# Kernel tuning notes

Measured on AMD Instinct MI355X. Metric: run time of the kernel, lower is better.

## Reference

```python
import jax, jax.numpy as jnp
import numpy as np

B, S, D, H, DFF = 2, 2048, 768, 12, 3072
DH = D // H
EPS = 1e-5


def _ln(x, g, b):
    m = jnp.mean(x, axis=-1, keepdims=True)
    v = jnp.mean((x - m) ** 2, axis=-1, keepdims=True)
    return (x - m) * jax.lax.rsqrt(v + EPS) * g + b


def setup_inputs() -> dict:
    key = jax.random.key(0)
    ks = jax.random.split(key, 13)
    sd = 1.0 / np.sqrt(D)
    sf = 1.0 / np.sqrt(DFF)
    return {
        "x": jax.random.normal(ks[0], (B, S, D), jnp.float32),
        "Wq": jax.random.uniform(ks[1], (D, D), jnp.float32, -sd, sd),
        "bq": jnp.zeros((D,), jnp.float32),
        "Wk": jax.random.uniform(ks[2], (D, D), jnp.float32, -sd, sd),
        "bk": jnp.zeros((D,), jnp.float32),
        "Wv": jax.random.uniform(ks[3], (D, D), jnp.float32, -sd, sd),
        "bv": jnp.zeros((D,), jnp.float32),
        "Wo": jax.random.uniform(ks[4], (D, D), jnp.float32, -sd, sd),
        "bo": jnp.zeros((D,), jnp.float32),
        "W1": jax.random.uniform(ks[5], (D, DFF), jnp.float32, -sd, sd),
        "b1": jnp.zeros((DFF,), jnp.float32),
        "W2": jax.random.uniform(ks[6], (DFF, D), jnp.float32, -sf, sf),
        "b2": jnp.zeros((D,), jnp.float32),
        "g1": jnp.ones((D,), jnp.float32),
        "be1": jnp.zeros((D,), jnp.float32),
        "g2": jnp.ones((D,), jnp.float32),
        "be2": jnp.zeros((D,), jnp.float32),
    }


def reference(x, Wq, bq, Wk, bk, Wv, bv, Wo, bo, W1, b1, W2, b2, g1, be1, g2, be2):
    # QKV projections, then split heads: [B,S,D] -> [B,H,S,DH]
    def heads(t):
        return t.reshape(B, S, H, DH).transpose(0, 2, 1, 3)
    Q = heads(x @ Wq + bq)
    K = heads(x @ Wk + bk)
    V = heads(x @ Wv + bv)
    # Per-head loop in original == batched-over-heads attention here (same math)
    scores = jnp.einsum("bhqd,bhkd->bhqk", Q, K) / np.sqrt(DH)
    attn = jax.nn.softmax(scores, axis=-1)  # [B,H,S,S] -- dominant intermediate
    ctx = jnp.einsum("bhqk,bhkd->bhqd", attn, V)
    ctx = ctx.transpose(0, 2, 1, 3).reshape(B, S, D)  # concat heads
    x = x + (ctx @ Wo + bo)
    x = _ln(x, g1, be1)
    ffn = (jax.nn.gelu(x @ W1 + b1, approximate=False)) @ W2 + b2
    x = _ln(x + ffn, g2, be2)
    return x
```

## Files before the change

kernel.cpp:

```cpp
#include <hip/hip_runtime.h>
#include <math.h>

#define BB 2
#define SS 2048
#define DD 768
#define HH 12
#define DHH 64
#define DFFN 3072
#define MTOK (BB*SS)

typedef __attribute__((ext_vector_type(8))) __bf16 bf16x8;
typedef __attribute__((ext_vector_type(4))) float f32x4;

__device__ __forceinline__ unsigned short f2bf(float f) {
    unsigned int b = __builtin_bit_cast(unsigned int, f);
    b += 0x7FFFu + ((b >> 16) & 1u);
    return (unsigned short)(b >> 16);
}

__device__ __forceinline__ void gload_lds16(const void* g, void* l) {
    __builtin_amdgcn_global_load_lds((const __attribute__((address_space(1))) unsigned int*)g,
                                     (__attribute__((address_space(3))) unsigned int*)l,
                                     16, 0, 0);
}

template <int ACT, int OBF>
__global__ __launch_bounds__(256) void gemm_mfma(const unsigned short* __restrict__ A,
                                                 const unsigned short* __restrict__ Bt,
                                                 const float* __restrict__ bias,
                                                 void* __restrict__ Cout,
                                                 int M, int N, int K) {
    __shared__ unsigned short As[128 * 64];
    __shared__ unsigned short Bs[128 * 64];
    const int tid = threadIdx.x;
    const int lane = tid & 63;
    const int w = tid >> 6;
    const int l15 = lane & 15, l4 = lane >> 4;
    const int m0 = blockIdx.x * 128;
    const int n0 = blockIdx.y * 128;
    const int wr = (w >> 1) * 64;
    const int wc = (w & 1) * 64;

    f32x4 acc[4][4] = {};

    int srow[4], scd[4];
#pragma unroll
    for (int i = 0; i < 4; ++i) {
        int s = w * 256 + i * 64 + lane;
        srow[i] = s >> 3;
        scd[i] = (((s & 7) ^ (srow[i] & 7))) * 8;
    }

    for (int k0 = 0; k0 < K; k0 += 64) {
        __syncthreads();
#pragma unroll
        for (int i = 0; i < 4; ++i) {
            const unsigned short* gA = A + (size_t)(m0 + srow[i]) * K + k0 + scd[i];
            gload_lds16(gA, &As[(w * 256 + i * 64) * 8]);
        }
#pragma unroll
        for (int i = 0; i < 4; ++i) {
            const unsigned short* gB = Bt + (size_t)(n0 + srow[i]) * K + k0 + scd[i];
            gload_lds16(gB, &Bs[(w * 256 + i * 64) * 8]);
        }
        __syncthreads();
#pragma unroll
        for (int ks = 0; ks < 2; ++ks) {
            bf16x8 af[4], bfr[4];
#pragma unroll
            for (int m = 0; m < 4; ++m) {
                int r = wr + m * 16 + l15;
                int c = (ks * 4 + l4) ^ (r & 7);
                af[m] = *(const bf16x8*)&As[(r * 8 + c) * 8];
            }
#pragma unroll
            for (int n = 0; n < 4; ++n) {
                int r = wc + n * 16 + l15;
                int c = (ks * 4 + l4) ^ (r & 7);
                bfr[n] = *(const bf16x8*)&Bs[(r * 8 + c) * 8];
            }
#pragma unroll
            for (int m = 0; m < 4; ++m)
#pragma unroll
                for (int n = 0; n < 4; ++n)
                    acc[m][n] = __builtin_amdgcn_mfma_f32_16x16x32_bf16(af[m], bfr[n], acc[m][n], 0, 0, 0);
        }
    }

#pragma unroll
    for (int n = 0; n < 4; ++n) {
        int col = n0 + wc + n * 16 + l15;
        float bv = bias[col];
#pragma unroll
        for (int m = 0; m < 4; ++m) {
#pragma unroll
            for (int r = 0; r < 4; ++r) {
                int row = m0 + wr + m * 16 + l4 * 4 + r;
                float v = acc[m][n][r] + bv;
                if (ACT) v = 0.5f * v * (1.0f + erff(v * 0.70710678118654752f));
                if (OBF) ((unsigned short*)Cout)[(size_t)row * N + col] = f2bf(v);
                else     ((float*)Cout)[(size_t)row * N + col] = v;
            }
        }
    }
}

__global__ __launch_bounds__(256) void attn_mfma(const unsigned short* __restrict__ QKV,
                                                 const unsigned short* __restrict__ Vt,
                                                 unsigned short* __restrict__ Ctx) {
    __shared__ unsigned short Ks[64 * 64];
    __shared__ unsigned short Vs[64 * 64];
    __shared__ unsigned short Ps[4 * 1024];
    const int tid = threadIdx.x;
    const int lane = tid & 63;
    const int w = tid >> 6;
    const int l15 = lane & 15, l4 = lane >> 4;
    const int bh = blockIdx.y;
    const int b = bh / HH, h = bh % HH;
    const int q0 = blockIdx.x * 64;
    unsigned short* pw = Ps + w * 1024;

    bf16x8 qf[2];
    {
        int qr = b * SS + q0 + w * 16 + l15;
        const unsigned short* qp = QKV + (size_t)qr * 2304 + h * 64 + l4 * 8;
        qf[0] = *(const bf16x8*)qp;
        qf[1] = *(const bf16x8*)(qp + 32);
    }

    f32x4 oacc[4] = {};
    float m_run[4], l_run[4];
#pragma unroll
    for (int r = 0; r < 4; ++r) { m_run[r] = -1e30f; l_run[r] = 0.0f; }

    int arow[2], acd[2];
#pragma unroll
    for (int i = 0; i < 2; ++i) {
        int s = w * 128 + i * 64 + lane;
        arow[i] = s >> 3;
        acd[i] = ((s & 7) ^ (arow[i] & 7)) * 8;
    }

    for (int kt = 0; kt < SS / 64; ++kt) {
        const int k0 = kt * 64;
        __syncthreads();
#pragma unroll
        for (int i = 0; i < 2; ++i) {
            const unsigned short* gK = QKV + (size_t)(b * SS + k0 + arow[i]) * 2304 + DD + h * 64 + acd[i];
            gload_lds16(gK, &Ks[(w * 128 + i * 64) * 8]);
        }
#pragma unroll
        for (int i = 0; i < 2; ++i) {
            const unsigned short* gV = Vt + (size_t)(bh * 64 + arow[i]) * SS + k0 + acd[i];
            gload_lds16(gV, &Vs[(w * 128 + i * 64) * 8]);
        }
        __syncthreads();

        f32x4 s4[4] = {};
#pragma unroll
        for (int ks = 0; ks < 2; ++ks) {
#pragma unroll
            for (int n = 0; n < 4; ++n) {
                int r = n * 16 + l15;
                int c = (ks * 4 + l4) ^ (r & 7);
                bf16x8 kf = *(const bf16x8*)&Ks[(r * 8 + c) * 8];
                s4[n] = __builtin_amdgcn_mfma_f32_16x16x32_bf16(qf[ks], kf, s4[n], 0, 0, 0);
            }
        }

        float p[4][4];
        float corr[4];
#pragma unroll
        for (int r = 0; r < 4; ++r) {
            float mt = fmaxf(fmaxf(s4[0][r], s4[1][r]), fmaxf(s4[2][r], s4[3][r])) * 0.125f;
#pragma unroll
            for (int off = 1; off < 16; off <<= 1) mt = fmaxf(mt, __shfl_xor(mt, off));
            float mn = fmaxf(m_run[r], mt);
            corr[r] = __expf(m_run[r] - mn);
            float rs = 0.0f;
#pragma unroll
            for (int n = 0; n < 4; ++n) {
                float pv = __expf(s4[n][r] * 0.125f - mn);
                p[n][r] = pv; rs += pv;
            }
#pragma unroll
            for (int off = 1; off < 16; off <<= 1) rs += __shfl_xor(rs, off);
            l_run[r] = l_run[r] * corr[r] + rs;
            m_run[r] = mn;
        }
#pragma unroll
        for (int n = 0; n < 4; ++n)
#pragma unroll
            for (int r = 0; r < 4; ++r) oacc[n][r] *= corr[r];

#pragma unroll
        for (int n = 0; n < 4; ++n) {
            int col = n * 16 + l15;
#pragma unroll
            for (int r = 0; r < 4; ++r) {
                int q = l4 * 4 + r;
                int byte = q * 128 + (((col >> 3) ^ (q & 7)) * 16) + (col & 7) * 2;
                *(unsigned short*)((char*)pw + byte) = f2bf(p[n][r]);
            }
        }

#pragma unroll
        for (int ks = 0; ks < 2; ++ks) {
            int cpa = (ks * 4 + l4) ^ (l15 & 7);
            bf16x8 pa = *(const bf16x8*)((const char*)pw + l15 * 128 + cpa * 16);
#pragma unroll
            for (int n = 0; n < 4; ++n) {
                int r = n * 16 + l15;
                int c = (ks * 4 + l4) ^ (r & 7);
                bf16x8 vf = *(const bf16x8*)&Vs[(r * 8 + c) * 8];
                oacc[n] = __builtin_amdgcn_mfma_f32_16x16x32_bf16(pa, vf, oacc[n], 0, 0, 0);
            }
        }
    }

#pragma unroll
    for (int n = 0; n < 4; ++n) {
        int col = h * 64 + n * 16 + l15;
#pragma unroll
        for (int r = 0; r < 4; ++r) {
            int q = b * SS + q0 + w * 16 + l4 * 4 + r;
            Ctx[(size_t)q * DD + col] = f2bf(oacc[n][r] / l_run[r]);
        }
    }
}

__global__ __launch_bounds__(256) void v_transpose(const unsigned short* __restrict__ QKV,
                                                   unsigned short* __restrict__ Vt) {
    __shared__ unsigned short t[64][66];
    const int tid = threadIdx.x;
    const int bh = blockIdx.y, b = bh / HH, h = bh % HH;
    const int s0 = blockIdx.x * 64;
    const int c = tid & 63, r0 = tid >> 6;
#pragma unroll
    for (int i = 0; i < 16; ++i) {
        int r = i * 4 + r0;
        t[r][c] = QKV[(size_t)(b * SS + s0 + r) * 2304 + 1536 + h * 64 + c];
    }
    __syncthreads();
#pragma unroll
    for (int i = 0; i < 16; ++i) {
        int r = i * 4 + r0;
        Vt[((size_t)bh * 64 + r) * SS + s0 + c] = t[c][r];
    }
}

__global__ __launch_bounds__(256) void wtrans(const float* __restrict__ W,
                                              unsigned short* __restrict__ Wt,
                                              int K, int N, int rowoff) {
    __shared__ float t[32][33];
    const int tid = threadIdx.x;
    const int k0 = blockIdx.x * 32, n0 = blockIdx.y * 32;
    const int c = tid & 31, r0 = tid >> 5;
#pragma unroll
    for (int i = 0; i < 4; ++i) {
        int r = i * 8 + r0;
        t[r][c] = W[(size_t)(k0 + r) * N + n0 + c];
    }
    __syncthreads();
#pragma unroll
    for (int i = 0; i < 4; ++i) {
        int r = i * 8 + r0;
        Wt[(size_t)(rowoff + n0 + r) * K + k0 + c] = f2bf(t[c][r]);
    }
}

__global__ __launch_bounds__(256) void f2b_vec(const float* __restrict__ in,
                                               unsigned short* __restrict__ out, int n4) {
    int i = blockIdx.x * 256 + threadIdx.x;
    if (i < n4) {
        float4 v = ((const float4*)in)[i];
        unsigned long long pk = (unsigned long long)f2bf(v.x)
                              | ((unsigned long long)f2bf(v.y) << 16)
                              | ((unsigned long long)f2bf(v.z) << 32)
                              | ((unsigned long long)f2bf(v.w) << 48);
        ((unsigned long long*)out)[i] = pk;
    }
}

__global__ __launch_bounds__(256) void bias_concat(const float* __restrict__ q,
                                                   const float* __restrict__ k,
                                                   const float* __restrict__ v,
                                                   float* __restrict__ o) {
    int i = blockIdx.x * 256 + threadIdx.x;
    if (i < DD) { o[i] = q[i]; o[DD + i] = k[i]; o[2 * DD + i] = v[i]; }
}

template <int WB>
__global__ __launch_bounds__(256) void add_ln(const float* __restrict__ a,
                                              const float* __restrict__ bsrc,
                                              const float* __restrict__ g,
                                              const float* __restrict__ be,
                                              float* __restrict__ outf,
                                              unsigned short* __restrict__ outb) {
    const int row = blockIdx.x;
    const int tid = threadIdx.x;
    float x[3];
    float s = 0.0f, s2 = 0.0f;
#pragma unroll
    for (int i = 0; i < 3; ++i) {
        int c = tid + i * 256;
        float v = a[(size_t)row * DD + c] + bsrc[(size_t)row * DD + c];
        x[i] = v; s += v; s2 += v * v;
    }
#pragma unroll
    for (int off = 32; off; off >>= 1) {
        s += __shfl_down(s, off);
        s2 += __shfl_down(s2, off);
    }
    __shared__ float ws[8];
    const int wid = tid >> 6, lane = tid & 63;
    if (lane == 0) { ws[wid] = s; ws[4 + wid] = s2; }
    __syncthreads();
    if (tid == 0) {
        ws[0] = ws[0] + ws[1] + ws[2] + ws[3];
        ws[4] = ws[4] + ws[5] + ws[6] + ws[7];
    }
    __syncthreads();
    const float mean = ws[0] * (1.0f / DD);
    const float var = ws[4] * (1.0f / DD) - mean * mean;
    const float inv = rsqrtf(var + 1e-5f);
#pragma unroll
    for (int i = 0; i < 3; ++i) {
        int c = tid + i * 256;
        float res = (x[i] - mean) * inv * g[c] + be[c];
        outf[(size_t)row * DD + c] = res;
        if (WB) outb[(size_t)row * DD + c] = f2bf(res);
    }
}

extern "C" void kernel_launch(void* const* d_in, const int* in_sizes, int n_in,
                              void* d_out, int out_size, void* d_ws, size_t ws_size,
                              hipStream_t stream) {
    const float* x   = (const float*)d_in[0];
    const float* Wq  = (const float*)d_in[1];
    const float* bq  = (const float*)d_in[2];
    const float* Wk  = (const float*)d_in[3];
    const float* bk  = (const float*)d_in[4];
    const float* Wv  = (const float*)d_in[5];
    const float* bv  = (const float*)d_in[6];
    const float* Wo  = (const float*)d_in[7];
    const float* bo  = (const float*)d_in[8];
    const float* W1  = (const float*)d_in[9];
    const float* b1  = (const float*)d_in[10];
    const float* W2  = (const float*)d_in[11];
    const float* b2  = (const float*)d_in[12];
    const float* g1  = (const float*)d_in[13];
    const float* be1 = (const float*)d_in[14];
    const float* g2  = (const float*)d_in[15];
    const float* be2 = (const float*)d_in[16];
    float* out = (float*)d_out;

    char* w8 = (char*)d_ws;
    unsigned short* QKV = (unsigned short*)w8;
    unsigned short* Vt  = (unsigned short*)(w8 + 18874368);
    unsigned short* Hff = (unsigned short*)w8;
    char* p = w8 + 25165824;
    unsigned short* Ctxb  = (unsigned short*)p; p += 6291456;
    unsigned short* xb    = (unsigned short*)p; p += 6291456;
    unsigned short* Wqkvt = (unsigned short*)p; p += 3538944;
    unsigned short* Wot   = (unsigned short*)p; p += 1179648;
    unsigned short* W1t   = (unsigned short*)p; p += 4718592;
    unsigned short* W2t   = (unsigned short*)p; p += 4718592;
    float* bqkv = (float*)p; p += 9216 + 256;
    float* Proj = (float*)p; p += 12582912;
    float* X2   = (float*)p; p += 12582912;

    dim3 blk(256);

    f2b_vec<<<dim3(3072), blk, 0, stream>>>(x, xb, MTOK * DD / 4);
    wtrans<<<dim3(24, 24), blk, 0, stream>>>(Wq, Wqkvt, DD, DD, 0);
    wtrans<<<dim3(24, 24), blk, 0, stream>>>(Wk, Wqkvt, DD, DD, DD);
    wtrans<<<dim3(24, 24), blk, 0, stream>>>(Wv, Wqkvt, DD, DD, 2 * DD);
    wtrans<<<dim3(24, 24), blk, 0, stream>>>(Wo, Wot, DD, DD, 0);
    wtrans<<<dim3(24, 96), blk, 0, stream>>>(W1, W1t, DD, DFFN, 0);
    wtrans<<<dim3(96, 24), blk, 0, stream>>>(W2, W2t, DFFN, DD, 0);
    bias_concat<<<dim3(3), blk, 0, stream>>>(bq, bk, bv, bqkv);

    gemm_mfma<0, 1><<<dim3(32, 18), blk, 0, stream>>>(xb, Wqkvt, bqkv, QKV, MTOK, 3 * DD, DD);
    v_transpose<<<dim3(32, 24), blk, 0, stream>>>(QKV, Vt);
    attn_mfma<<<dim3(32, 24), blk, 0, stream>>>(QKV, Vt, Ctxb);
    gemm_mfma<0, 0><<<dim3(32, 6), blk, 0, stream>>>(Ctxb, Wot, bo, Proj, MTOK, DD, DD);
    add_ln<1><<<dim3(MTOK), blk, 0, stream>>>(x, Proj, g1, be1, X2, xb);
    gemm_mfma<1, 1><<<dim3(32, 24), blk, 0, stream>>>(xb, W1t, b1, Hff, MTOK, DFFN, DD);
    gemm_mfma<0, 0><<<dim3(32, 6), blk, 0, stream>>>(Hff, W2t, b2, Proj, MTOK, DD, DFFN);
    add_ln<0><<<dim3(MTOK), blk, 0, stream>>>(X2, Proj, g2, be2, out, nullptr);
}
```

Measured before the change: 381.9 us.

## Use 32x32 MFMA flash attention with register P; split-K output GEMMs

The attention kernel is rewritten to use 32x32x16 MFMA with 32 query rows per wave and 128 queries per block. Computing S^T lets the P matrix stay in registers, moved between lanes with cross-half shuffles instead of an LDS round-trip, and softmax uses exp2 with the scale folded in. The Wo and W2 GEMMs are split along K into two launches writing separate fp32 partials. Those partials are summed with the bias inside a new three-input add+LayerNorm kernel. The split aims to fill more CUs for the narrow N=768 GEMMs, at the cost of an extra partial-buffer write and read.

```diff
diff --git a/kernel.cpp b/kernel.cpp
--- a/kernel.cpp
+++ b/kernel.cpp
@@ -11,6 +11,7 @@
 
 typedef __attribute__((ext_vector_type(8))) __bf16 bf16x8;
 typedef __attribute__((ext_vector_type(4))) float f32x4;
+typedef __attribute__((ext_vector_type(16))) float f32x16;
 
 __device__ __forceinline__ unsigned short f2bf(float f) {
     unsigned int b = __builtin_bit_cast(unsigned int, f);
@@ -29,7 +30,7 @@
                                                  const unsigned short* __restrict__ Bt,
                                                  const float* __restrict__ bias,
                                                  void* __restrict__ Cout,
-                                                 int M, int N, int K) {
+                                                 int M, int N, int ldA, int ldB, int Klen) {
     __shared__ unsigned short As[128 * 64];
     __shared__ unsigned short Bs[128 * 64];
     const int tid = threadIdx.x;
@@ -51,16 +52,16 @@
         scd[i] = (((s & 7) ^ (srow[i] & 7))) * 8;
     }
 
-    for (int k0 = 0; k0 < K; k0 += 64) {
+    for (int k0 = 0; k0 < Klen; k0 += 64) {
         __syncthreads();
 #pragma unroll
         for (int i = 0; i < 4; ++i) {
-            const unsigned short* gA = A + (size_t)(m0 + srow[i]) * K + k0 + scd[i];
+            const unsigned short* gA = A + (size_t)(m0 + srow[i]) * ldA + k0 + scd[i];
             gload_lds16(gA, &As[(w * 256 + i * 64) * 8]);
         }
 #pragma unroll
         for (int i = 0; i < 4; ++i) {
-            const unsigned short* gB = Bt + (size_t)(n0 + srow[i]) * K + k0 + scd[i];
+            const unsigned short* gB = Bt + (size_t)(n0 + srow[i]) * ldB + k0 + scd[i];
             gload_lds16(gB, &Bs[(w * 256 + i * 64) * 8]);
         }
         __syncthreads();
@@ -90,7 +91,7 @@
 #pragma unroll
     for (int n = 0; n < 4; ++n) {
         int col = n0 + wc + n * 16 + l15;
-        float bv = bias[col];
+        float bv = bias ? bias[col] : 0.0f;
 #pragma unroll
         for (int m = 0; m < 4; ++m) {
 #pragma unroll
@@ -105,33 +106,32 @@
     }
 }
 
-__global__ __launch_bounds__(256) void attn_mfma(const unsigned short* __restrict__ QKV,
-                                                 const unsigned short* __restrict__ Vt,
-                                                 unsigned short* __restrict__ Ctx) {
+__global__ __launch_bounds__(256) void attn_mfma2(const unsigned short* __restrict__ QKV,
+                                                  const unsigned short* __restrict__ Vt,
+                                                  unsigned short* __restrict__ Ctx) {
     __shared__ unsigned short Ks[64 * 64];
     __shared__ unsigned short Vs[64 * 64];
-    __shared__ unsigned short Ps[4 * 1024];
     const int tid = threadIdx.x;
     const int lane = tid & 63;
     const int w = tid >> 6;
-    const int l15 = lane & 15, l4 = lane >> 4;
+    const int l31 = lane & 31;
+    const int hi = lane >> 5;
     const int bh = blockIdx.y;
     const int b = bh / HH, h = bh % HH;
-    const int q0 = blockIdx.x * 64;
-    unsigned short* pw = Ps + w * 1024;
-
-    bf16x8 qf[2];
+    const int q0 = blockIdx.x * 128 + w * 32;
+    const float CLOG = 0.18033688011112042f;
+
+    bf16x8 qf[4];
     {
-        int qr = b * SS + q0 + w * 16 + l15;
-        const unsigned short* qp = QKV + (size_t)qr * 2304 + h * 64 + l4 * 8;
+        const unsigned short* qp = QKV + (size_t)(b * SS + q0 + l31) * 2304 + h * 64 + hi * 8;
         qf[0] = *(const bf16x8*)qp;
-        qf[1] = *(const bf16x8*)(qp + 32);
-    }
-
-    f32x4 oacc[4] = {};
-    float m_run[4], l_run[4];
-#pragma unroll
-    for (int r = 0; r < 4; ++r) { m_run[r] = -1e30f; l_run[r] = 0.0f; }
+        qf[1] = *(const bf16x8*)(qp + 16);
+        qf[2] = *(const bf16x8*)(qp + 32);
+        qf[3] = *(const bf16x8*)(qp + 48);
+    }
+
+    f32x16 oacc[2] = {};
+    float m_run = -1e30f, l_run = 0.0f;
 
     int arow[2], acd[2];
 #pragma unroll
@@ -156,75 +156,93 @@
         }
         __syncthreads();
 
-        f32x4 s4[4] = {};
-#pragma unroll
-        for (int ks = 0; ks < 2; ++ks) {
-#pragma unroll
-            for (int n = 0; n < 4; ++n) {
-                int r = n * 16 + l15;
-                int c = (ks * 4 + l4) ^ (r & 7);
-                bf16x8 kf = *(const bf16x8*)&Ks[(r * 8 + c) * 8];
-                s4[n] = __builtin_amdgcn_mfma_f32_16x16x32_bf16(qf[ks], kf, s4[n], 0, 0, 0);
-            }
-        }
-
-        float p[4][4];
-        float corr[4];
-#pragma unroll
-        for (int r = 0; r < 4; ++r) {
-            float mt = fmaxf(fmaxf(s4[0][r], s4[1][r]), fmaxf(s4[2][r], s4[3][r])) * 0.125f;
-#pragma unroll
-            for (int off = 1; off < 16; off <<= 1) mt = fmaxf(mt, __shfl_xor(mt, off));
-            float mn = fmaxf(m_run[r], mt);
-            corr[r] = __expf(m_run[r] - mn);
-            float rs = 0.0f;
-#pragma unroll
-            for (int n = 0; n < 4; ++n) {
-                float pv = __expf(s4[n][r] * 0.125f - mn);
-                p[n][r] = pv; rs += pv;
-            }
-#pragma unroll
-            for (int off = 1; off < 16; off <<= 1) rs += __shfl_xor(rs, off);
-            l_run[r] = l_run[r] * corr[r] + rs;
-            m_run[r] = mn;
-        }
-#pragma unroll
-        for (int n = 0; n < 4; ++n)
-#pragma unroll
-            for (int r = 0; r < 4; ++r) oacc[n][r] *= corr[r];
-
-#pragma unroll
-        for (int n = 0; n < 4; ++n) {
-            int col = n * 16 + l15;
-#pragma unroll
-            for (int r = 0; r < 4; ++r) {
-                int q = l4 * 4 + r;
-                int byte = q * 128 + (((col >> 3) ^ (q & 7)) * 16) + (col & 7) * 2;
-                *(unsigned short*)((char*)pw + byte) = f2bf(p[n][r]);
-            }
-        }
-
-#pragma unroll
-        for (int ks = 0; ks < 2; ++ks) {
-            int cpa = (ks * 4 + l4) ^ (l15 & 7);
-            bf16x8 pa = *(const bf16x8*)((const char*)pw + l15 * 128 + cpa * 16);
-#pragma unroll
-            for (int n = 0; n < 4; ++n) {
-                int r = n * 16 + l15;
-                int c = (ks * 4 + l4) ^ (r & 7);
-                bf16x8 vf = *(const bf16x8*)&Vs[(r * 8 + c) * 8];
-                oacc[n] = __builtin_amdgcn_mfma_f32_16x16x32_bf16(pa, vf, oacc[n], 0, 0, 0);
-            }
-        }
-    }
-
-#pragma unroll
-    for (int n = 0; n < 4; ++n) {
-        int col = h * 64 + n * 16 + l15;
-#pragma unroll
-        for (int r = 0; r < 4; ++r) {
-            int q = b * SS + q0 + w * 16 + l4 * 4 + r;
-            Ctx[(size_t)q * DD + col] = f2bf(oacc[n][r] / l_run[r]);
+        f32x16 st[2] = {};
+#pragma unroll
+        for (int t = 0; t < 2; ++t) {
+#pragma unroll
+            for (int ks = 0; ks < 4; ++ks) {
+                int row = 32 * t + l31;
+                int ch = (2 * ks + hi) ^ (row & 7);
+                bf16x8 kf = *(const bf16x8*)&Ks[(row * 8 + ch) * 8];
+                st[t] = __builtin_amdgcn_mfma_f32_32x32x16_bf16(kf, qf[ks], st[t], 0, 0, 0);
+            }
+        }
+
+        float pmax = st[0][0];
+#pragma unroll
+        for (int r = 1; r < 16; ++r) pmax = fmaxf(pmax, st[0][r]);
+#pragma unroll
+        for (int r = 0; r < 16; ++r) pmax = fmaxf(pmax, st[1][r]);
+        pmax = fmaxf(pmax, __shfl_xor(pmax, 32));
+        pmax *= CLOG;
+        const float mn = fmaxf(m_run, pmax);
+        const float corr = exp2f(m_run - mn);
+
+        unsigned int Wn[2][4][2];
+        float rs = 0.0f;
+#pragma unroll
+        for (int t = 0; t < 2; ++t) {
+#pragma unroll
+            for (int blk = 0; blk < 4; ++blk) {
+                float pa = exp2f(fmaf(st[t][4 * blk + 0], CLOG, -mn));
+                float pb = exp2f(fmaf(st[t][4 * blk + 1], CLOG, -mn));
+                float pc = exp2f(fmaf(st[t][4 * blk + 2], CLOG, -mn));
+                float pd = exp2f(fmaf(st[t][4 * blk + 3], CLOG, -mn));
+                rs += (pa + pb) + (pc + pd);
+                Wn[t][blk][0] = (unsigned int)f2bf(pa) | ((unsigned int)f2bf(pb) << 16);
+                Wn[t][blk][1] = (unsigned int)f2bf(pc) | ((unsigned int)f2bf(pd) << 16);
+            }
+        }
+        rs += __shfl_xor(rs, 32);
+        l_run = l_run * corr + rs;
+        m_run = mn;
+
+#pragma unroll
+        for (int d = 0; d < 2; ++d)
+#pragma unroll
+            for (int r = 0; r < 16; ++r) oacc[d][r] *= corr;
+
+        unsigned int PW[2][4][2];
+#pragma unroll
+        for (int t = 0; t < 2; ++t)
+#pragma unroll
+            for (int blk = 0; blk < 4; ++blk)
+#pragma unroll
+                for (int u = 0; u < 2; ++u) PW[t][blk][u] = __shfl_xor(Wn[t][blk][u], 32);
+
+        const bool h1 = (hi == 1);
+#pragma unroll
+        for (int t = 0; t < 2; ++t) {
+#pragma unroll
+            for (int ks2 = 0; ks2 < 2; ++ks2) {
+                union { unsigned int u[4]; bf16x8 v; } pu;
+                pu.u[0] = h1 ? PW[t][2 * ks2 + 1][0] : Wn[t][2 * ks2][0];
+                pu.u[1] = h1 ? PW[t][2 * ks2 + 1][1] : Wn[t][2 * ks2][1];
+                pu.u[2] = h1 ? Wn[t][2 * ks2 + 1][0] : PW[t][2 * ks2][0];
+                pu.u[3] = h1 ? Wn[t][2 * ks2 + 1][1] : PW[t][2 * ks2][1];
+#pragma unroll
+                for (int d = 0; d < 2; ++d) {
+                    int row = 32 * d + l31;
+                    int ch = (4 * t + 2 * ks2 + hi) ^ (row & 7);
+                    bf16x8 vf = *(const bf16x8*)&Vs[(row * 8 + ch) * 8];
+                    oacc[d] = __builtin_amdgcn_mfma_f32_32x32x16_bf16(vf, pu.v, oacc[d], 0, 0, 0);
+                }
+            }
+        }
+    }
+
+    const float inv = 1.0f / l_run;
+    unsigned short* cp = Ctx + (size_t)(b * SS + q0 + l31) * DD + h * 64;
+#pragma unroll
+    for (int d = 0; d < 2; ++d) {
+#pragma unroll
+        for (int blk = 0; blk < 4; ++blk) {
+            unsigned long long pk =
+                  (unsigned long long)f2bf(oacc[d][4 * blk + 0] * inv)
+                | ((unsigned long long)f2bf(oacc[d][4 * blk + 1] * inv) << 16)
+                | ((unsigned long long)f2bf(oacc[d][4 * blk + 2] * inv) << 32)
+                | ((unsigned long long)f2bf(oacc[d][4 * blk + 3] * inv) << 48);
+            *(unsigned long long*)(cp + 32 * d + 8 * blk + 4 * hi) = pk;
         }
     }
 }
@@ -291,12 +309,14 @@
 }
 
 template <int WB>
-__global__ __launch_bounds__(256) void add_ln(const float* __restrict__ a,
-                                              const float* __restrict__ bsrc,
-                                              const float* __restrict__ g,
-                                              const float* __restrict__ be,
-                                              float* __restrict__ outf,
-                                              unsigned short* __restrict__ outb) {
+__global__ __launch_bounds__(256) void add_ln3(const float* __restrict__ a,
+                                               const float* __restrict__ p1,
+                                               const float* __restrict__ p2,
+                                               const float* __restrict__ bias,
+                                               const float* __restrict__ g,
+                                               const float* __restrict__ be,
+                                               float* __restrict__ outf,
+                                               unsigned short* __restrict__ outb) {
     const int row = blockIdx.x;
     const int tid = threadIdx.x;
     float x[3];
@@ -304,7 +324,8 @@
 #pragma unroll
     for (int i = 0; i < 3; ++i) {
         int c = tid + i * 256;
-        float v = a[(size_t)row * DD + c] + bsrc[(size_t)row * DD + c];
+        size_t idx = (size_t)row * DD + c;
+        float v = a[idx] + p1[idx] + p2[idx] + bias[c];
         x[i] = v; s += v; s2 += v * v;
     }
 #pragma unroll
@@ -357,18 +378,18 @@
 
     char* w8 = (char*)d_ws;
     unsigned short* QKV = (unsigned short*)w8;
+    unsigned short* Hff = (unsigned short*)w8;
     unsigned short* Vt  = (unsigned short*)(w8 + 18874368);
-    unsigned short* Hff = (unsigned short*)w8;
-    char* p = w8 + 25165824;
-    unsigned short* Ctxb  = (unsigned short*)p; p += 6291456;
-    unsigned short* xb    = (unsigned short*)p; p += 6291456;
-    unsigned short* Wqkvt = (unsigned short*)p; p += 3538944;
-    unsigned short* Wot   = (unsigned short*)p; p += 1179648;
-    unsigned short* W1t   = (unsigned short*)p; p += 4718592;
-    unsigned short* W2t   = (unsigned short*)p; p += 4718592;
-    float* bqkv = (float*)p; p += 9216 + 256;
-    float* Proj = (float*)p; p += 12582912;
-    float* X2   = (float*)p; p += 12582912;
+    unsigned short* Ctxb  = (unsigned short*)(w8 + 25165824);
+    unsigned short* xb    = (unsigned short*)(w8 + 31457280);
+    unsigned short* Wqkvt = (unsigned short*)(w8 + 37748736);
+    unsigned short* Wot   = (unsigned short*)(w8 + 41287680);
+    unsigned short* W1t   = (unsigned short*)(w8 + 42467328);
+    unsigned short* W2t   = (unsigned short*)(w8 + 47185920);
+    float* bqkv = (float*)(w8 + 51904512);
+    float* Pa   = (float*)(w8 + 51916800);
+    float* Pb   = (float*)(w8 + 64499712);
+    float* X2   = (float*)(w8 + 77082624);
 
     dim3 blk(256);
 
@@ -381,12 +402,20 @@
     wtrans<<<dim3(96, 24), blk, 0, stream>>>(W2, W2t, DFFN, DD, 0);
     bias_concat<<<dim3(3), blk, 0, stream>>>(bq, bk, bv, bqkv);
 
-    gemm_mfma<0, 1><<<dim3(32, 18), blk, 0, stream>>>(xb, Wqkvt, bqkv, QKV, MTOK, 3 * DD, DD);
+    gemm_mfma<0, 1><<<dim3(32, 18), blk, 0, stream>>>(xb, Wqkvt, bqkv, QKV,
+                                                      MTOK, 3 * DD, DD, DD, DD);
     v_transpose<<<dim3(32, 24), blk, 0, stream>>>(QKV, Vt);
-    attn_mfma<<<dim3(32, 24), blk, 0, stream>>>(QKV, Vt, Ctxb);
-    gemm_mfma<0, 0><<<dim3(32, 6), blk, 0, stream>>>(Ctxb, Wot, bo, Proj, MTOK, DD, DD);
-    add_ln<1><<<dim3(MTOK), blk, 0, stream>>>(x, Proj, g1, be1, X2, xb);
-    gemm_mfma<1, 1><<<dim3(32, 24), blk, 0, stream>>>(xb, W1t, b1, Hff, MTOK, DFFN, DD);
-    gemm_mfma<0, 0><<<dim3(32, 6), blk, 0, stream>>>(Hff, W2t, b2, Proj, MTOK, DD, DFFN);
-    add_ln<0><<<dim3(MTOK), blk, 0, stream>>>(X2, Proj, g2, be2, out, nullptr);
-}
+    attn_mfma2<<<dim3(SS / 128, BB * HH), blk, 0, stream>>>(QKV, Vt, Ctxb);
+    gemm_mfma<0, 0><<<dim3(32, 6), blk, 0, stream>>>(Ctxb, Wot, nullptr, Pa,
+                                                     MTOK, DD, DD, DD, 384);
+    gemm_mfma<0, 0><<<dim3(32, 6), blk, 0, stream>>>(Ctxb + 384, Wot + 384, nullptr, Pb,
+                                                     MTOK, DD, DD, DD, 384);
+    add_ln3<1><<<dim3(MTOK), blk, 0, stream>>>(x, Pa, Pb, bo, g1, be1, X2, xb);
+    gemm_mfma<1, 1><<<dim3(32, 24), blk, 0, stream>>>(xb, W1t, b1, Hff,
+                                                      MTOK, DFFN, DD, DD, DD);
+    gemm_mfma<0, 0><<<dim3(32, 6), blk, 0, stream>>>(Hff, W2t, nullptr, Pa,
+                                                     MTOK, DD, DFFN, DFFN, 1536);
+    gemm_mfma<0, 0><<<dim3(32, 6), blk, 0, stream>>>(Hff + 1536, W2t + 1536, nullptr, Pb,
+                                                     MTOK, DD, DFFN, DFFN, 1536);
+    add_ln3<0><<<dim3(MTOK), blk, 0, stream>>>(X2, Pa, Pb, b2, g2, be2, out, nullptr);
+}
```

After: 387.2 us. About the same (+1.4%).
